# Performance work log

Hardware: AMD Instinct MI355X
Metric: run time of the kernel (lower is better)

Reference implementation:

```python
import jax, jax.numpy as jnp
import numpy as np

B = 1024
H = 2048  # hidden_size
D = 2048  # input_size

def setup_inputs() -> dict:
    key = jax.random.key(0)
    k1, k2, k3, k4 = jax.random.split(key, 4)
    x = jax.random.normal(k1, (B, D), dtype=jnp.float32)
    h = jax.random.normal(k2, (B, H), dtype=jnp.float32)
    c = jax.random.normal(k3, (B, H), dtype=jnp.float32)
    W = jax.random.normal(k4, (D + H, 4 * H), dtype=jnp.float32) * 0.02
    return {"x": x, "h": h, "c": c, "W": W}

def reference(x, h, c, W):
    # merged = cat([x, h], dim=1); weighted = merged @ W
    merged = jnp.concatenate([x, h], axis=1)          # (B, D+H)
    weighted = merged @ W                             # (B, 4H)
    hid = W.shape[1] // 4
    c_f, c_i, c_g, c_o = jnp.split(weighted, 4, axis=1)
    c_new = c * jax.nn.sigmoid(c_f) + jax.nn.sigmoid(c_i) * jnp.tanh(c_g)
    h_new = jax.nn.sigmoid(c_o) * jnp.tanh(c_new)
    return h_new
```

## Files before the change

### kernel.cpp

```cpp
#include <hip/hip_runtime.h>

typedef __attribute__((ext_vector_type(4))) float          f32x4;
typedef __attribute__((ext_vector_type(8))) __bf16         bf16x8;
typedef __attribute__((ext_vector_type(8))) unsigned short u16x8;

#define B_  1024
#define D_  2048
#define H_  2048
#define K_  4096
#define N_  8192

__device__ __forceinline__ unsigned short f2bf_rne(float f) {
  unsigned u = __builtin_bit_cast(unsigned, f);
  u += 0x7fffu + ((u >> 16) & 1u);
  return (unsigned short)(u >> 16);
}

__device__ __forceinline__ float sigf(float x) {
  return 1.f / (1.f + __expf(-x));
}
__device__ __forceinline__ float tanhf_(float x) {
  float ax = fabsf(x);
  float t  = __expf(-2.f * ax);
  float r  = (1.f - t) / (1.f + t);
  return (x < 0.f) ? -r : r;
}

typedef const __attribute__((address_space(1))) unsigned int* gptr_t;
typedef __attribute__((address_space(3))) unsigned int*       lptr_t;
__device__ __forceinline__ void gl_lds16(const void* g, void* l) {
  __builtin_amdgcn_global_load_lds((gptr_t)g, (lptr_t)l, 16, 0, 0);
}

__global__ __launch_bounds__(256) void k_convert_merged(
    const float* __restrict__ x, const float* __restrict__ h,
    unsigned short* __restrict__ merged) {
  int tid = blockIdx.x * 256 + threadIdx.x;
  int e0  = tid * 8;
  int b   = e0 >> 12;
  int col = e0 & 4095;
  const float* src = (col < D_) ? (x + (size_t)b * D_ + col)
                                : (h + (size_t)b * H_ + (col - D_));
  f32x4 v0 = *(const f32x4*)src;
  f32x4 v1 = *(const f32x4*)(src + 4);
  u16x8 o;
  o[0] = f2bf_rne(v0[0]); o[1] = f2bf_rne(v0[1]);
  o[2] = f2bf_rne(v0[2]); o[3] = f2bf_rne(v0[3]);
  o[4] = f2bf_rne(v1[0]); o[5] = f2bf_rne(v1[1]);
  o[6] = f2bf_rne(v1[2]); o[7] = f2bf_rne(v1[3]);
  *(u16x8*)(merged + e0) = o;
}

__global__ __launch_bounds__(256) void k_transpose_w(
    const float* __restrict__ W, unsigned short* __restrict__ Wt) {
  __shared__ float lt[64 * 64];
  char* lbase = (char*)lt;
  const int t   = threadIdx.x;
  const int g   = blockIdx.x & 3;
  const int jb  = blockIdx.x >> 2;
  const int n0s = g * 2048 + jb * 64;
  const int k0  = blockIdx.y * 64;
#pragma unroll
  for (int i = 0; i < 4; ++i) {
    int kk = (t >> 4) + i * 16;
    int nn = (t & 15) * 4;
    f32x4 v = *(const f32x4*)&W[(size_t)(k0 + kk) * N_ + n0s + nn];
    int by = (kk * 256 + nn * 4) ^ (((kk >> 3) & 7) << 4);
    *(f32x4*)(lbase + by) = v;
  }
  __syncthreads();
#pragma unroll
  for (int i = 0; i < 2; ++i) {
    int jl = (t >> 3) + i * 32;
    int kc = (t & 7) * 8;
    u16x8 o;
#pragma unroll
    for (int jj = 0; jj < 8; ++jj) {
      int k  = kc + jj;
      int by = (k * 256 + jl * 4) ^ (((k >> 3) & 7) << 4);
      o[jj] = f2bf_rne(*(const float*)(lbase + by));
    }
    int j    = jb * 64 + jl;
    int nrow = ((j >> 4) * 64) + g * 16 + (j & 15);
    *(u16x8*)&Wt[(size_t)nrow * K_ + k0 + kc] = o;
  }
}

#define TM 128
#define TN 128
#define TK 64

__global__ __launch_bounds__(512, 4) void k_gemm(
    const unsigned short* __restrict__ A,
    const unsigned short* __restrict__ Bt,
    const float* __restrict__ c,
    float* __restrict__ out) {
  __shared__ unsigned short As[TM * TK];
  __shared__ unsigned short Bs[TN * TK];
  const int t    = threadIdx.x;
  const int bx   = blockIdx.x;
  const int by   = blockIdx.y;
  const int w    = t >> 6;
  const int lane = t & 63;
  const int wr   = w >> 1, wc = w & 1;
  const int ln15 = lane & 15, kq = lane >> 4;

  const int srow  = w * 8 + (lane >> 3);
  const int chunk = (lane & 7) * 16;

  const char* gA = (const char*)A  + (size_t)(by * TM + srow) * (K_ * 2) + chunk;
  const char* gB = (const char*)Bt + (size_t)(bx * TN + srow) * (K_ * 2) + chunk;
  char* lA = (char*)As + t * 16;
  char* lB = (char*)Bs + t * 16;
  const size_t half = (size_t)64 * (K_ * 2);

  f32x4 acc[2][4] = {};

  for (int kt = 0; kt < K_ / TK; ++kt) {
    const int gofs = kt * (TK * 2);
    gl_lds16(gA + gofs,        lA);
    gl_lds16(gA + half + gofs, lA + 8192);
    gl_lds16(gB + gofs,        lB);
    gl_lds16(gB + half + gofs, lB + 8192);
    __syncthreads();
#pragma unroll
    for (int ks = 0; ks < 2; ++ks) {
      bf16x8 a[2], b[4];
#pragma unroll
      for (int mi = 0; mi < 2; ++mi)
        a[mi] = *(const bf16x8*)((const char*)As +
                 (wr * 32 + mi * 16 + ln15) * (TK * 2) + ks * 64 + kq * 16);
#pragma unroll
      for (int ni = 0; ni < 4; ++ni)
        b[ni] = *(const bf16x8*)((const char*)Bs +
                 (wc * 64 + ni * 16 + ln15) * (TK * 2) + ks * 64 + kq * 16);
#pragma unroll
      for (int mi = 0; mi < 2; ++mi)
#pragma unroll
        for (int ni = 0; ni < 4; ++ni)
          acc[mi][ni] = __builtin_amdgcn_mfma_f32_16x16x32_bf16(
              a[mi], b[ni], acc[mi][ni], 0, 0, 0);
    }
    __syncthreads();
  }

  const int row0 = by * TM + wr * 32 + kq * 4;
  const int j    = (bx * 2 + wc) * 16 + ln15;
#pragma unroll
  for (int mi = 0; mi < 2; ++mi)
#pragma unroll
    for (int r = 0; r < 4; ++r) {
      int row   = row0 + mi * 16 + r;
      float fg  = acc[mi][0][r];
      float ig  = acc[mi][1][r];
      float gg  = acc[mi][2][r];
      float og  = acc[mi][3][r];
      float cv  = c[(size_t)row * H_ + j];
      float cn  = cv * sigf(fg) + sigf(ig) * tanhf_(gg);
      out[(size_t)row * H_ + j] = sigf(og) * tanhf_(cn);
    }
}

extern "C" void kernel_launch(void* const* d_in, const int* in_sizes, int n_in,
                              void* d_out, int out_size, void* d_ws, size_t ws_size,
                              hipStream_t stream) {
  (void)in_sizes; (void)n_in; (void)out_size; (void)ws_size;
  const float* x = (const float*)d_in[0];
  const float* h = (const float*)d_in[1];
  const float* c = (const float*)d_in[2];
  const float* W = (const float*)d_in[3];
  float* out = (float*)d_out;

  char* ws = (char*)d_ws;
  unsigned short* merged = (unsigned short*)ws;
  unsigned short* Wt     = (unsigned short*)(ws + (size_t)8  * 1024 * 1024);

  k_convert_merged<<<2048, 256, 0, stream>>>(x, h, merged);
  k_transpose_w<<<dim3(128, 64), 256, 0, stream>>>(W, Wt);
  k_gemm<<<dim3(N_ / TN, B_ / TM), 512, 0, stream>>>(merged, Wt, c, out);
}
```

Before: 319.8 us.

## Triple-buffer GEMM K-loop with larger 128x256 tiles and swizzled LDS

Rewrites the fused GEMM+LSTM kernel to use a 128x256 block tile with 8 waves each computing 64x64, and a three-stage LDS ring buffer with direct global-to-LDS loads issued two K-steps ahead. Waits use explicit vmcnt counts so loads overlap MFMA work, the LDS layout is XOR-swizzled to reduce bank conflicts, and MFMA issue gets raised priority. This aims to hide global load latency and raise per-wave arithmetic intensity. The cost is larger LDS use and more accumulator registers, so occupancy drops to 2 blocks/CU, and the grid shrinks to 256 blocks.

```diff
diff --git a/kernel.cpp b/kernel.cpp
--- a/kernel.cpp
+++ b/kernel.cpp
@@ -86,68 +86,122 @@
   }
 }
 
-#define TM 128
-#define TN 128
-#define TK 64
-
-__global__ __launch_bounds__(512, 4) void k_gemm(
+#define NT 64
+#define ABUF 16384
+#define BBUF 32768
+#define BUFSZ (ABUF + BBUF)
+
+__global__ __launch_bounds__(512, 2) void k_gemm(
     const unsigned short* __restrict__ A,
     const unsigned short* __restrict__ Bt,
     const float* __restrict__ c,
     float* __restrict__ out) {
-  __shared__ unsigned short As[TM * TK];
-  __shared__ unsigned short Bs[TN * TK];
+  __shared__ char smem[3 * BUFSZ];
+  char* LA0 = smem;               char* LB0 = smem + ABUF;
+  char* LA1 = smem + BUFSZ;       char* LB1 = smem + BUFSZ + ABUF;
+  char* LA2 = smem + 2 * BUFSZ;   char* LB2 = smem + 2 * BUFSZ + ABUF;
+
   const int t    = threadIdx.x;
   const int bx   = blockIdx.x;
   const int by   = blockIdx.y;
   const int w    = t >> 6;
   const int lane = t & 63;
-  const int wr   = w >> 1, wc = w & 1;
-  const int ln15 = lane & 15, kq = lane >> 4;
-
-  const int srow  = w * 8 + (lane >> 3);
-  const int chunk = (lane & 7) * 16;
-
-  const char* gA = (const char*)A  + (size_t)(by * TM + srow) * (K_ * 2) + chunk;
-  const char* gB = (const char*)Bt + (size_t)(bx * TN + srow) * (K_ * 2) + chunk;
-  char* lA = (char*)As + t * 16;
-  char* lB = (char*)Bs + t * 16;
-  const size_t half = (size_t)64 * (K_ * 2);
-
-  f32x4 acc[2][4] = {};
-
-  for (int kt = 0; kt < K_ / TK; ++kt) {
-    const int gofs = kt * (TK * 2);
-    gl_lds16(gA + gofs,        lA);
-    gl_lds16(gA + half + gofs, lA + 8192);
-    gl_lds16(gB + gofs,        lB);
-    gl_lds16(gB + half + gofs, lB + 8192);
-    __syncthreads();
-#pragma unroll
-    for (int ks = 0; ks < 2; ++ks) {
-      bf16x8 a[2], b[4];
-#pragma unroll
-      for (int mi = 0; mi < 2; ++mi)
-        a[mi] = *(const bf16x8*)((const char*)As +
-                 (wr * 32 + mi * 16 + ln15) * (TK * 2) + ks * 64 + kq * 16);
-#pragma unroll
-      for (int ni = 0; ni < 4; ++ni)
-        b[ni] = *(const bf16x8*)((const char*)Bs +
-                 (wc * 64 + ni * 16 + ln15) * (TK * 2) + ks * 64 + kq * 16);
-#pragma unroll
-      for (int mi = 0; mi < 2; ++mi)
-#pragma unroll
-        for (int ni = 0; ni < 4; ++ni)
-          acc[mi][ni] = __builtin_amdgcn_mfma_f32_16x16x32_bf16(
-              a[mi], b[ni], acc[mi][ni], 0, 0, 0);
-    }
-    __syncthreads();
+  const int wr   = w >> 2, wc = w & 3;
+  const int ln15 = lane & 15, kq = (lane >> 4) & 3;
+
+  const int srow = t >> 3;
+  const int scb  = (t & 7) * 16;
+  const int ssw  = ((srow & 7) << 4);
+  const int scbx = scb ^ ssw;
+  const char* sA0 = (const char*)A  + ((size_t)(by * 128 + srow)      * K_) * 2 + scbx;
+  const char* sA1 = (const char*)A  + ((size_t)(by * 128 + srow + 64) * K_) * 2 + scbx;
+  const char* sB0 = (const char*)Bt + ((size_t)(bx * 256 + srow)       * K_) * 2 + scbx;
+  const char* sB1 = (const char*)Bt + ((size_t)(bx * 256 + srow + 64)  * K_) * 2 + scbx;
+  const char* sB2 = (const char*)Bt + ((size_t)(bx * 256 + srow + 128) * K_) * 2 + scbx;
+  const char* sB3 = (const char*)Bt + ((size_t)(bx * 256 + srow + 192) * K_) * 2 + scbx;
+  const int ldst = t * 16;
+
+#define STAGE(LA, LB, KO) do {                         \
+    gl_lds16(sA0 + (KO), (LA) + ldst);                 \
+    gl_lds16(sA1 + (KO), (LA) + 8192 + ldst);          \
+    gl_lds16(sB0 + (KO), (LB) + ldst);                 \
+    gl_lds16(sB1 + (KO), (LB) + 8192 + ldst);          \
+    gl_lds16(sB2 + (KO), (LB) + 16384 + ldst);         \
+    gl_lds16(sB3 + (KO), (LB) + 24576 + ldst);         \
+  } while (0)
+
+  const int swz  = (ln15 & 7) << 4;
+  const int aRow = wr * 8192 + ln15 * 128;
+  const int bRow = wc * 8192 + ln15 * 128;
+
+  f32x4 acc[4][4] = {};
+
+#define COMPUTE(LA, LB) do {                                             \
+    _Pragma("unroll")                                                    \
+    for (int ks = 0; ks < 2; ++ks) {                                     \
+      const int cb = (ks * 64 + kq * 16) ^ swz;                          \
+      bf16x8 a0 = *(const bf16x8*)((LA) + aRow          + cb);           \
+      bf16x8 a1 = *(const bf16x8*)((LA) + aRow + 2048   + cb);           \
+      bf16x8 a2 = *(const bf16x8*)((LA) + aRow + 4096   + cb);           \
+      bf16x8 a3 = *(const bf16x8*)((LA) + aRow + 6144   + cb);           \
+      bf16x8 b0 = *(const bf16x8*)((LB) + bRow          + cb);           \
+      bf16x8 b1 = *(const bf16x8*)((LB) + bRow + 2048   + cb);           \
+      bf16x8 b2 = *(const bf16x8*)((LB) + bRow + 4096   + cb);           \
+      bf16x8 b3 = *(const bf16x8*)((LB) + bRow + 6144   + cb);           \
+      __builtin_amdgcn_s_setprio(1);                                     \
+      acc[0][0] = __builtin_amdgcn_mfma_f32_16x16x32_bf16(a0, b0, acc[0][0], 0, 0, 0); \
+      acc[0][1] = __builtin_amdgcn_mfma_f32_16x16x32_bf16(a0, b1, acc[0][1], 0, 0, 0); \
+      acc[0][2] = __builtin_amdgcn_mfma_f32_16x16x32_bf16(a0, b2, acc[0][2], 0, 0, 0); \
+      acc[0][3] = __builtin_amdgcn_mfma_f32_16x16x32_bf16(a0, b3, acc[0][3], 0, 0, 0); \
+      acc[1][0] = __builtin_amdgcn_mfma_f32_16x16x32_bf16(a1, b0, acc[1][0], 0, 0, 0); \
+      acc[1][1] = __builtin_amdgcn_mfma_f32_16x16x32_bf16(a1, b1, acc[1][1], 0, 0, 0); \
+      acc[1][2] = __builtin_amdgcn_mfma_f32_16x16x32_bf16(a1, b2, acc[1][2], 0, 0, 0); \
+      acc[1][3] = __builtin_amdgcn_mfma_f32_16x16x32_bf16(a1, b3, acc[1][3], 0, 0, 0); \
+      acc[2][0] = __builtin_amdgcn_mfma_f32_16x16x32_bf16(a2, b0, acc[2][0], 0, 0, 0); \
+      acc[2][1] = __builtin_amdgcn_mfma_f32_16x16x32_bf16(a2, b1, acc[2][1], 0, 0, 0); \
+      acc[2][2] = __builtin_amdgcn_mfma_f32_16x16x32_bf16(a2, b2, acc[2][2], 0, 0, 0); \
+      acc[2][3] = __builtin_amdgcn_mfma_f32_16x16x32_bf16(a2, b3, acc[2][3], 0, 0, 0); \
+      acc[3][0] = __builtin_amdgcn_mfma_f32_16x16x32_bf16(a3, b0, acc[3][0], 0, 0, 0); \
+      acc[3][1] = __builtin_amdgcn_mfma_f32_16x16x32_bf16(a3, b1, acc[3][1], 0, 0, 0); \
+      acc[3][2] = __builtin_amdgcn_mfma_f32_16x16x32_bf16(a3, b2, acc[3][2], 0, 0, 0); \
+      acc[3][3] = __builtin_amdgcn_mfma_f32_16x16x32_bf16(a3, b3, acc[3][3], 0, 0, 0); \
+      __builtin_amdgcn_s_setprio(0);                                     \
+    }                                                                    \
+  } while (0)
+
+#define WAITBAR(NSTR) do {                                   \
+    asm volatile("s_waitcnt vmcnt(" NSTR ")" ::: "memory");  \
+    __builtin_amdgcn_sched_barrier(0);                       \
+    __builtin_amdgcn_s_barrier();                            \
+    __builtin_amdgcn_sched_barrier(0);                       \
+  } while (0)
+
+  STAGE(LA0, LB0, 0);
+  STAGE(LA1, LB1, 128);
+
+  for (int ktb = 0; ktb < 63; ktb += 3) {
+    const size_t ko = (size_t)(ktb + 2) * 128;
+    WAITBAR("6");
+    STAGE(LA2, LB2, ko);
+    COMPUTE(LA0, LB0);
+    WAITBAR("6");
+    STAGE(LA0, LB0, ko + 128);
+    COMPUTE(LA1, LB1);
+    WAITBAR("6");
+    if (ktb < 60) STAGE(LA1, LB1, ko + 256);
+    COMPUTE(LA2, LB2);
   }
-
-  const int row0 = by * TM + wr * 32 + kq * 4;
-  const int j    = (bx * 2 + wc) * 16 + ln15;
-#pragma unroll
-  for (int mi = 0; mi < 2; ++mi)
+  WAITBAR("0");
+  COMPUTE(LA0, LB0);
+
+#undef STAGE
+#undef COMPUTE
+#undef WAITBAR
+
+  const int row0 = by * 128 + wr * 64 + kq * 4;
+  const int j    = (bx * 4 + wc) * 16 + ln15;
+#pragma unroll
+  for (int mi = 0; mi < 4; ++mi)
 #pragma unroll
     for (int r = 0; r < 4; ++r) {
       int row   = row0 + mi * 16 + r;
@@ -177,5 +231,5 @@
 
   k_convert_merged<<<2048, 256, 0, stream>>>(x, h, merged);
   k_transpose_w<<<dim3(128, 64), 256, 0, stream>>>(W, Wt);
-  k_gemm<<<dim3(N_ / TN, B_ / TM), 512, 0, stream>>>(merged, Wt, c, out);
-}
+  k_gemm<<<dim3(32, 8), 512, 0, stream>>>(merged, Wt, c, out);
+}
```

Result: faster. 283.7 us (-11.3%).
